# Performance work log

Measured on AMD Instinct MI355X. Metric: run time of the kernel, lower is better.

Reference implementation:

```python
import jax, jax.numpy as jnp
import numpy as np

# Static ragged group sizes (cav_num per sample); sum = 28 rows of x.
RECORD_LEN = np.array([2, 3, 4, 5, 3, 2, 4, 5], dtype=np.int64)
C, W, H = 256, 48, 176


def setup_inputs() -> dict:
    key = jax.random.key(0)
    n_total = int(RECORD_LEN.sum())
    x = jax.random.normal(key, (n_total, C, W, H), dtype=jnp.float32)
    return {
        "x": x,
        "record_len": jnp.asarray(RECORD_LEN),
        "fusion_method": 1,
    }


def _attentive_group(xx, sqrt_dim):
    # xx: [n, C, W, H] -> tokens over spatial positions: [S, n, C], S = W*H
    n = xx.shape[0]
    q = xx.reshape(n, C, W * H).transpose(2, 0, 1)          # [S, n, C]
    score = jnp.einsum('snc,smc->snm', q, q) / sqrt_dim     # [S, n, n]
    attn = jax.nn.softmax(score, axis=-1)
    ctx = jnp.einsum('snm,smc->snc', attn, q)               # [S, n, C]
    # original keeps only ego agent (row 0): [0, ...].unsqueeze(0)
    return ctx[:, 0, :].T.reshape(1, C, W, H)


def reference(x, record_len, fusion_method):
    # fusion_method == 1 -> attentiveFusion (per-group bmm-softmax-bmm over cav dim)
    rl = np.asarray(record_len)
    offs = np.concatenate([[0], np.cumsum(rl)])
    sqrt_dim = np.float32(np.sqrt(x.shape[1]))
    # Python loop over the small fixed set of ragged groups (8), as in the original.
    outs = [_attentive_group(x[int(offs[i]):int(offs[i + 1])], sqrt_dim)
            for i in range(len(rl))]
    return jnp.concatenate(outs, axis=0)                    # [batch, C, W, H]
```

## Files before the change

### kernel.cpp

```cpp
#include <hip/hip_runtime.h>


#define C_DIM 256
#define S_DIM (48 * 176)
#define CS ((long long)C_DIM * S_DIM)
#define TS 64
#define NTILES (S_DIM / TS)
#define NSLICE 16
#define CPS (C_DIM / NSLICE)

template <int N>
__device__ __forceinline__ void att_group(const float* __restrict__ x,
                                          float* __restrict__ out,
                                          float4* __restrict__ pd,
                                          int off, int b, int stile, int tid) {
    const int g  = tid & 15;
    const int cy = tid >> 4;
    const int s  = stile * TS + g * 4;
    const float* xb    = x + (long long)off * CS + s;
    const float* cbase = xb + (long long)(cy * CPS) * S_DIM;

    float dx[N], dy[N], dz[N], dw[N];
#pragma unroll
    for (int j = 0; j < N; ++j) { dx[j] = dy[j] = dz[j] = dw[j] = 0.f; }

#pragma unroll 4
    for (int c = 0; c < CPS; ++c) {
        const float* p = cbase + (long long)c * S_DIM;
        float4 v0 = *(const float4*)p;
        dx[0] = fmaf(v0.x, v0.x, dx[0]);
        dy[0] = fmaf(v0.y, v0.y, dy[0]);
        dz[0] = fmaf(v0.z, v0.z, dz[0]);
        dw[0] = fmaf(v0.w, v0.w, dw[0]);
#pragma unroll
        for (int j = 1; j < N; ++j) {
            float4 v = *(const float4*)(p + (long long)j * CS);
            dx[j] = fmaf(v0.x, v.x, dx[j]);
            dy[j] = fmaf(v0.y, v.y, dy[j]);
            dz[j] = fmaf(v0.z, v.z, dz[j]);
            dw[j] = fmaf(v0.w, v.w, dw[j]);
        }
    }

#pragma unroll
    for (int j = 0; j < N; ++j)
        pd[(cy * 5 + j) * 16 + g] = make_float4(dx[j], dy[j], dz[j], dw[j]);
    __syncthreads();

#pragma unroll
    for (int step = 8; step >= 1; step >>= 1) {
        if (cy < step) {
#pragma unroll
            for (int j = 0; j < N; ++j) {
                float4 a = pd[(cy * 5 + j) * 16 + g];
                float4 c2 = pd[((cy + step) * 5 + j) * 16 + g];
                a.x += c2.x; a.y += c2.y; a.z += c2.z; a.w += c2.w;
                pd[(cy * 5 + j) * 16 + g] = a;
            }
        }
        __syncthreads();
    }

    float dv[4][N], wv[4][N];
#pragma unroll
    for (int j = 0; j < N; ++j) {
        float4 t = pd[j * 16 + g];
        dv[0][j] = t.x; dv[1][j] = t.y; dv[2][j] = t.z; dv[3][j] = t.w;
    }
#pragma unroll
    for (int k = 0; k < 4; ++k) {
        float m = dv[k][0];
#pragma unroll
        for (int j = 1; j < N; ++j) m = fmaxf(m, dv[k][j]);
        float sum = 0.f;
#pragma unroll
        for (int j = 0; j < N; ++j) {
            wv[k][j] = __expf((dv[k][j] - m) * 0.0625f);
            sum += wv[k][j];
        }
        float inv = 1.f / sum;
#pragma unroll
        for (int j = 0; j < N; ++j) wv[k][j] *= inv;
    }

    float* ob = out + (long long)b * CS + s + (long long)(cy * CPS) * S_DIM;
#pragma unroll 4
    for (int c = 0; c < CPS; ++c) {
        const float* p = cbase + (long long)c * S_DIM;
        float4 acc = make_float4(0.f, 0.f, 0.f, 0.f);
#pragma unroll
        for (int j = 0; j < N; ++j) {
            float4 v = *(const float4*)(p + (long long)j * CS);
            acc.x = fmaf(wv[0][j], v.x, acc.x);
            acc.y = fmaf(wv[1][j], v.y, acc.y);
            acc.z = fmaf(wv[2][j], v.z, acc.z);
            acc.w = fmaf(wv[3][j], v.w, acc.w);
        }
        *(float4*)(ob + (long long)c * S_DIM) = acc;
    }
}

__global__ __launch_bounds__(256) void att_fusion_kernel(const float* __restrict__ x,
                                                         float* __restrict__ out) {
    __shared__ float4 pd[NSLICE * 5 * 16];
    const int stile = blockIdx.x;
    const int b     = blockIdx.y;
    const int tid   = (int)threadIdx.x;
    switch (b) {
        case 0: att_group<2>(x, out, pd,  0, 0, stile, tid); break;
        case 1: att_group<3>(x, out, pd,  2, 1, stile, tid); break;
        case 2: att_group<4>(x, out, pd,  5, 2, stile, tid); break;
        case 3: att_group<5>(x, out, pd,  9, 3, stile, tid); break;
        case 4: att_group<3>(x, out, pd, 14, 4, stile, tid); break;
        case 5: att_group<2>(x, out, pd, 17, 5, stile, tid); break;
        case 6: att_group<4>(x, out, pd, 19, 6, stile, tid); break;
        case 7: att_group<5>(x, out, pd, 23, 7, stile, tid); break;
    }
}

extern "C" void kernel_launch(void* const* d_in, const int* in_sizes, int n_in,
                              void* d_out, int out_size, void* d_ws, size_t ws_size,
                              hipStream_t stream) {
    const float* x = (const float*)d_in[0];
    float* out = (float*)d_out;
    dim3 grid(NTILES, 8);
    dim3 block(256);
    hipLaunchKernelGGL(att_fusion_kernel, grid, block, 0, stream, x, out);
}
```

Measured before the change: 390.4 us.

## Keep group inputs in registers and reduce dot products with wave shuffles

Shrinks the spatial tile to 16 and spreads all 256 channels across the block's threads. Each thread loads its x values once into registers and reuses them for both the score dot products and the weighted sum, so the second global read of x goes away. The shared-memory tree reduction with multiple barriers is replaced by xor shuffles inside each wave plus one small shared-memory combine. The cost is higher register pressure and narrower 64-byte contiguous accesses per channel row.

```diff
diff --git a/kernel.cpp b/kernel.cpp
--- a/kernel.cpp
+++ b/kernel.cpp
@@ -4,69 +4,77 @@
 #define C_DIM 256
 #define S_DIM (48 * 176)
 #define CS ((long long)C_DIM * S_DIM)
-#define TS 64
+#define TS 16
 #define NTILES (S_DIM / TS)
-#define NSLICE 16
-#define CPS (C_DIM / NSLICE)
 
 template <int N>
 __device__ __forceinline__ void att_group(const float* __restrict__ x,
                                           float* __restrict__ out,
-                                          float4* __restrict__ pd,
+                                          float4* __restrict__ pdr,
                                           int off, int b, int stile, int tid) {
-    const int g  = tid & 15;
-    const int cy = tid >> 4;
-    const int s  = stile * TS + g * 4;
-    const float* xb    = x + (long long)off * CS + s;
-    const float* cbase = xb + (long long)(cy * CPS) * S_DIM;
+    const int q  = tid & 3;
+    const int cs = tid >> 2;
+    const int s  = stile * TS + q * 4;
+    const float* xb = x + (long long)off * CS + (long long)cs * S_DIM + s;
+
+    float4 v[4][N];
+#pragma unroll
+    for (int it = 0; it < 4; ++it) {
+#pragma unroll
+        for (int j = 0; j < N; ++j) {
+            v[it][j] = *(const float4*)(xb + (long long)j * CS
+                                           + (long long)(it * 64) * S_DIM);
+        }
+    }
 
     float dx[N], dy[N], dz[N], dw[N];
 #pragma unroll
     for (int j = 0; j < N; ++j) { dx[j] = dy[j] = dz[j] = dw[j] = 0.f; }
-
-#pragma unroll 4
-    for (int c = 0; c < CPS; ++c) {
-        const float* p = cbase + (long long)c * S_DIM;
-        float4 v0 = *(const float4*)p;
-        dx[0] = fmaf(v0.x, v0.x, dx[0]);
-        dy[0] = fmaf(v0.y, v0.y, dy[0]);
-        dz[0] = fmaf(v0.z, v0.z, dz[0]);
-        dw[0] = fmaf(v0.w, v0.w, dw[0]);
 #pragma unroll
-        for (int j = 1; j < N; ++j) {
-            float4 v = *(const float4*)(p + (long long)j * CS);
-            dx[j] = fmaf(v0.x, v.x, dx[j]);
-            dy[j] = fmaf(v0.y, v.y, dy[j]);
-            dz[j] = fmaf(v0.z, v.z, dz[j]);
-            dw[j] = fmaf(v0.w, v.w, dw[j]);
+    for (int it = 0; it < 4; ++it) {
+        const float4 v0 = v[it][0];
+#pragma unroll
+        for (int j = 0; j < N; ++j) {
+            dx[j] = fmaf(v0.x, v[it][j].x, dx[j]);
+            dy[j] = fmaf(v0.y, v[it][j].y, dy[j]);
+            dz[j] = fmaf(v0.z, v[it][j].z, dz[j]);
+            dw[j] = fmaf(v0.w, v[it][j].w, dw[j]);
         }
     }
 
 #pragma unroll
-    for (int j = 0; j < N; ++j)
-        pd[(cy * 5 + j) * 16 + g] = make_float4(dx[j], dy[j], dz[j], dw[j]);
+    for (int mask = 4; mask <= 32; mask <<= 1) {
+#pragma unroll
+        for (int j = 0; j < N; ++j) {
+            dx[j] += __shfl_xor(dx[j], mask);
+            dy[j] += __shfl_xor(dy[j], mask);
+            dz[j] += __shfl_xor(dz[j], mask);
+            dw[j] += __shfl_xor(dw[j], mask);
+        }
+    }
+
+    const int w = tid >> 6;
+    if ((tid & 63) < 4) {
+#pragma unroll
+        for (int j = 0; j < N; ++j)
+            pdr[(w * 4 + q) * 5 + j] = make_float4(dx[j], dy[j], dz[j], dw[j]);
+    }
     __syncthreads();
 
+    float dv[4][N];
 #pragma unroll
-    for (int step = 8; step >= 1; step >>= 1) {
-        if (cy < step) {
-#pragma unroll
-            for (int j = 0; j < N; ++j) {
-                float4 a = pd[(cy * 5 + j) * 16 + g];
-                float4 c2 = pd[((cy + step) * 5 + j) * 16 + g];
-                a.x += c2.x; a.y += c2.y; a.z += c2.z; a.w += c2.w;
-                pd[(cy * 5 + j) * 16 + g] = a;
-            }
-        }
-        __syncthreads();
+    for (int j = 0; j < N; ++j) {
+        float4 t0 = pdr[(0  + q) * 5 + j];
+        float4 t1 = pdr[(4  + q) * 5 + j];
+        float4 t2 = pdr[(8  + q) * 5 + j];
+        float4 t3 = pdr[(12 + q) * 5 + j];
+        dv[0][j] = t0.x + t1.x + t2.x + t3.x;
+        dv[1][j] = t0.y + t1.y + t2.y + t3.y;
+        dv[2][j] = t0.z + t1.z + t2.z + t3.z;
+        dv[3][j] = t0.w + t1.w + t2.w + t3.w;
     }
 
-    float dv[4][N], wv[4][N];
-#pragma unroll
-    for (int j = 0; j < N; ++j) {
-        float4 t = pd[j * 16 + g];
-        dv[0][j] = t.x; dv[1][j] = t.y; dv[2][j] = t.z; dv[3][j] = t.w;
-    }
+    float wt[4][N];
 #pragma unroll
     for (int k = 0; k < 4; ++k) {
         float m = dv[k][0];
@@ -75,46 +83,44 @@
         float sum = 0.f;
 #pragma unroll
         for (int j = 0; j < N; ++j) {
-            wv[k][j] = __expf((dv[k][j] - m) * 0.0625f);
-            sum += wv[k][j];
+            wt[k][j] = __expf((dv[k][j] - m) * 0.0625f);
+            sum += wt[k][j];
         }
         float inv = 1.f / sum;
 #pragma unroll
-        for (int j = 0; j < N; ++j) wv[k][j] *= inv;
+        for (int j = 0; j < N; ++j) wt[k][j] *= inv;
     }
 
-    float* ob = out + (long long)b * CS + s + (long long)(cy * CPS) * S_DIM;
-#pragma unroll 4
-    for (int c = 0; c < CPS; ++c) {
-        const float* p = cbase + (long long)c * S_DIM;
+    float* ob = out + (long long)b * CS + (long long)cs * S_DIM + s;
+#pragma unroll
+    for (int it = 0; it < 4; ++it) {
         float4 acc = make_float4(0.f, 0.f, 0.f, 0.f);
 #pragma unroll
         for (int j = 0; j < N; ++j) {
-            float4 v = *(const float4*)(p + (long long)j * CS);
-            acc.x = fmaf(wv[0][j], v.x, acc.x);
-            acc.y = fmaf(wv[1][j], v.y, acc.y);
-            acc.z = fmaf(wv[2][j], v.z, acc.z);
-            acc.w = fmaf(wv[3][j], v.w, acc.w);
+            acc.x = fmaf(wt[0][j], v[it][j].x, acc.x);
+            acc.y = fmaf(wt[1][j], v[it][j].y, acc.y);
+            acc.z = fmaf(wt[2][j], v[it][j].z, acc.z);
+            acc.w = fmaf(wt[3][j], v[it][j].w, acc.w);
         }
-        *(float4*)(ob + (long long)c * S_DIM) = acc;
+        *(float4*)(ob + (long long)(it * 64) * S_DIM) = acc;
     }
 }
 
 __global__ __launch_bounds__(256) void att_fusion_kernel(const float* __restrict__ x,
                                                          float* __restrict__ out) {
-    __shared__ float4 pd[NSLICE * 5 * 16];
+    __shared__ float4 pdr[16 * 5];
     const int stile = blockIdx.x;
     const int b     = blockIdx.y;
     const int tid   = (int)threadIdx.x;
     switch (b) {
-        case 0: att_group<2>(x, out, pd,  0, 0, stile, tid); break;
-        case 1: att_group<3>(x, out, pd,  2, 1, stile, tid); break;
-        case 2: att_group<4>(x, out, pd,  5, 2, stile, tid); break;
-        case 3: att_group<5>(x, out, pd,  9, 3, stile, tid); break;
-        case 4: att_group<3>(x, out, pd, 14, 4, stile, tid); break;
-        case 5: att_group<2>(x, out, pd, 17, 5, stile, tid); break;
-        case 6: att_group<4>(x, out, pd, 19, 6, stile, tid); break;
-        case 7: att_group<5>(x, out, pd, 23, 7, stile, tid); break;
+        case 0: att_group<2>(x, out, pdr,  0, 0, stile, tid); break;
+        case 1: att_group<3>(x, out, pdr,  2, 1, stile, tid); break;
+        case 2: att_group<4>(x, out, pdr,  5, 2, stile, tid); break;
+        case 3: att_group<5>(x, out, pdr,  9, 3, stile, tid); break;
+        case 4: att_group<3>(x, out, pdr, 14, 4, stile, tid); break;
+        case 5: att_group<2>(x, out, pdr, 17, 5, stile, tid); break;
+        case 6: att_group<4>(x, out, pdr, 19, 6, stile, tid); break;
+        case 7: att_group<5>(x, out, pdr, 23, 7, stile, tid); break;
     }
 }
 
```

After: 382.8 us. No clear change (-2.0%).
